# Performance work log

Measured on AMD Instinct MI355X. Metric: run time of the kernel, lower is better.

The kernel has to match this reference:

```python
import jax, jax.numpy as jnp
import numpy as np

B, I, O, K = 16384, 512, 64, 4


def setup_inputs() -> dict:
    key = jax.random.key(0)
    k1, k2, k3 = jax.random.split(key, 3)
    x = jax.random.normal(k1, (B, I), dtype=jnp.float32)
    weights = jax.random.normal(k2, (O, I), dtype=jnp.float32)
    # per-(o,i) Fourier coefficients, init like torch.randn * 0.1
    coefficients = jax.random.normal(k3, (O, I, 2 * K + 1), dtype=jnp.float32) * 0.1
    return {"x": x, "weights": weights, "coefficients": coefficients}


def reference(x, weights, coefficients):
    # x: [B, I]; weights: [O, I]; coefficients: [O, I, 2K+1]
    Kf = coefficients.shape[-1] // 2
    freqs = jnp.arange(1, Kf + 1, dtype=x.dtype)          # (k+1) for k in range(K)
    ang = x[:, :, None] * freqs                            # [B, I, K]
    sin_v = jnp.sin(ang)                                   # [B, I, K]
    cos_v = jnp.cos(ang)                                   # [B, I, K]
    c0 = coefficients[..., 0]                              # [O, I] constant term
    a = coefficients[..., 1::2]                            # [O, I, K] sin coeffs
    b = coefficients[..., 2::2]                            # [O, I, K] cos coeffs
    # out[b,o] = sum_i w[o,i] * (c0[o,i] + sum_k a*sin + b*cos)
    const = jnp.sum(weights * c0, axis=1)                  # [O]
    out = (const[None, :]
           + jnp.einsum('bik,oik->bo', sin_v, weights[:, :, None] * a)
           + jnp.einsum('bik,oik->bo', cos_v, weights[:, :, None] * b))
    return out
```

## Files before the change

kernel.cpp:

```cpp
#include <hip/hip_runtime.h>

#define B_ROWS 16384
#define I_DIM  512
#define O_DIM  64
#define NFEAT  8
#define W2_BYTES ((size_t)I_DIM * O_DIM * NFEAT * 2)

typedef _Float16 f16x8 __attribute__((ext_vector_type(8)));
typedef float    f32x4 __attribute__((ext_vector_type(4)));

__global__ __launch_bounds__(256) void prep_w2(const float* __restrict__ w,
                                               const float* __restrict__ coef,
                                               _Float16* __restrict__ w2) {
    int t = blockIdx.x * 256 + threadIdx.x;
    int i = t >> 6;
    int o = t & 63;
    float wv = w[o * I_DIM + i];
    const float* cp = coef + ((size_t)(o * I_DIM + i)) * 9;
    f16x8 v;
#pragma unroll
    for (int f = 0; f < 8; ++f) v[f] = (_Float16)(wv * cp[f + 1]);
    *reinterpret_cast<f16x8*>(w2 + (size_t)t * 8) = v;
}

__global__ __launch_bounds__(64) void prep_const(const float* __restrict__ w,
                                                 const float* __restrict__ coef,
                                                 float* __restrict__ cst) {
    int o = blockIdx.x;
    int l = threadIdx.x;
    float s = 0.f;
    for (int i = l; i < I_DIM; i += 64)
        s += w[o * I_DIM + i] * coef[((size_t)(o * I_DIM + i)) * 9];
#pragma unroll
    for (int off = 32; off; off >>= 1) s += __shfl_down(s, off, 64);
    if (l == 0) cst[o] = s;
}

__global__ __launch_bounds__(512) void fourier_main(const float* __restrict__ x,
                                                    const _Float16* __restrict__ w2,
                                                    const float* __restrict__ cst,
                                                    float* __restrict__ out) {
    __shared__ float red[4][64][64];

    const int tid   = threadIdx.x;
    const int wave  = tid >> 6;
    const int lane  = tid & 63;
    const int col16 = lane & 15;
    const int ig    = lane >> 4;
    const int rbase = blockIdx.x * 64;

    f32x4 acc[4][4] = {};
    const int i0 = wave * 64;

    const float* xr[4];
#pragma unroll
    for (int m = 0; m < 4; ++m)
        xr[m] = x + (size_t)(rbase + m * 16 + col16) * I_DIM;

    const f16x8* __restrict__ bbase = reinterpret_cast<const f16x8*>(w2);

    for (int s = 0; s < 16; ++s) {
        const int i = i0 + s * 4 + ig;

        f16x8 bf[4];
#pragma unroll
        for (int n = 0; n < 4; ++n) bf[n] = bbase[i * 64 + n * 16 + col16];

        float xv[4];
#pragma unroll
        for (int m = 0; m < 4; ++m) xv[m] = xr[m][i];

#pragma unroll
        for (int m = 0; m < 4; ++m) {
            float s1, c1;
            __sincosf(xv[m], &s1, &c1);
            const float tc = 2.f * c1;
            const float s2 = tc * s1;
            const float c2 = tc * c1 - 1.f;
            const float s3 = tc * s2 - s1;
            const float c3 = tc * c2 - c1;
            const float s4 = tc * s3 - s2;
            const float c4 = tc * c3 - c2;
            f16x8 af;
            af[0] = (_Float16)s1; af[1] = (_Float16)c1;
            af[2] = (_Float16)s2; af[3] = (_Float16)c2;
            af[4] = (_Float16)s3; af[5] = (_Float16)c3;
            af[6] = (_Float16)s4; af[7] = (_Float16)c4;
#pragma unroll
            for (int n = 0; n < 4; ++n)
                acc[m][n] = __builtin_amdgcn_mfma_f32_16x16x32_f16(af, bf[n], acc[m][n], 0, 0, 0);
        }
    }

    if (wave < 4) {
#pragma unroll
        for (int m = 0; m < 4; ++m)
#pragma unroll
            for (int n = 0; n < 4; ++n)
#pragma unroll
                for (int q = 0; q < 4; ++q)
                    red[wave][m * 16 + ig * 4 + q][n * 16 + col16] = acc[m][n][q];
    }
    __syncthreads();
    if (wave >= 4) {
#pragma unroll
        for (int m = 0; m < 4; ++m)
#pragma unroll
            for (int n = 0; n < 4; ++n)
#pragma unroll
                for (int q = 0; q < 4; ++q)
                    red[wave - 4][m * 16 + ig * 4 + q][n * 16 + col16] += acc[m][n][q];
    }
    __syncthreads();

    const float cv = cst[lane];
#pragma unroll
    for (int j = 0; j < 8; ++j) {
        const int r = wave + 8 * j;
        const int c = lane;
        float v = cv + red[0][r][c] + red[1][r][c] + red[2][r][c] + red[3][r][c];
        out[(size_t)(rbase + r) * 64 + c] = v;
    }
}

extern "C" void kernel_launch(void* const* d_in, const int* in_sizes, int n_in,
                              void* d_out, int out_size, void* d_ws, size_t ws_size,
                              hipStream_t stream) {
    const float* x    = (const float*)d_in[0];
    const float* w    = (const float*)d_in[1];
    const float* coef = (const float*)d_in[2];
    _Float16* w2  = (_Float16*)d_ws;
    float*    cst = (float*)((char*)d_ws + W2_BYTES);
    float*    out = (float*)d_out;

    hipLaunchKernelGGL(prep_w2,    dim3(128), dim3(256), 0, stream, w, coef, w2);
    hipLaunchKernelGGL(prep_const, dim3(64),  dim3(64),  0, stream, w, coef, cst);
    hipLaunchKernelGGL(fourier_main, dim3(B_ROWS / 64), dim3(512), 0, stream, x, w2, cst, out);
}
```

Baseline: 99.94 us.

## Stage x tile through shared memory with coalesced loads and prefetch weights

The main kernel now loads the block's 64x512 x tile with coalesced float4 global loads into registers. It writes the tile into a 128KB shared buffer in four row groups, and each wave reads its x values from shared memory instead of making strided per-row global loads. The loop order changes to row-group outer, with software prefetch of the next weight fragments. The reduction buffer reuses the x storage with padding. The prep kernels get coalesced reads and a wider reduction. The large shared allocation limits residency to one block per CU, and weight fragments are now reloaded for each row group, adding cache traffic.

```diff
diff --git a/kernel.cpp b/kernel.cpp
--- a/kernel.cpp
+++ b/kernel.cpp
@@ -13,34 +13,39 @@
                                                const float* __restrict__ coef,
                                                _Float16* __restrict__ w2) {
     int t = blockIdx.x * 256 + threadIdx.x;
-    int i = t >> 6;
-    int o = t & 63;
-    float wv = w[o * I_DIM + i];
-    const float* cp = coef + ((size_t)(o * I_DIM + i)) * 9;
+    int o = t >> 9;
+    int i = t & 511;
+    float wv = w[t];
+    const float* cp = coef + (size_t)t * 9;
     f16x8 v;
 #pragma unroll
     for (int f = 0; f < 8; ++f) v[f] = (_Float16)(wv * cp[f + 1]);
-    *reinterpret_cast<f16x8*>(w2 + (size_t)t * 8) = v;
+    *reinterpret_cast<f16x8*>(w2 + ((size_t)(i * 64 + o)) * 8) = v;
 }
 
-__global__ __launch_bounds__(64) void prep_const(const float* __restrict__ w,
-                                                 const float* __restrict__ coef,
-                                                 float* __restrict__ cst) {
+__global__ __launch_bounds__(256) void prep_const(const float* __restrict__ w,
+                                                  const float* __restrict__ coef,
+                                                  float* __restrict__ cst) {
     int o = blockIdx.x;
-    int l = threadIdx.x;
+    int t = threadIdx.x;
     float s = 0.f;
-    for (int i = l; i < I_DIM; i += 64)
+#pragma unroll
+    for (int i = t; i < I_DIM; i += 256)
         s += w[o * I_DIM + i] * coef[((size_t)(o * I_DIM + i)) * 9];
 #pragma unroll
     for (int off = 32; off; off >>= 1) s += __shfl_down(s, off, 64);
-    if (l == 0) cst[o] = s;
+    __shared__ float ps[4];
+    if ((t & 63) == 0) ps[t >> 6] = s;
+    __syncthreads();
+    if (t == 0) cst[o] = ps[0] + ps[1] + ps[2] + ps[3];
 }
 
-__global__ __launch_bounds__(512) void fourier_main(const float* __restrict__ x,
-                                                    const _Float16* __restrict__ w2,
-                                                    const float* __restrict__ cst,
-                                                    float* __restrict__ out) {
-    __shared__ float red[4][64][64];
+__global__ __launch_bounds__(512, 2) void fourier_main(const float* __restrict__ x,
+                                                       const _Float16* __restrict__ w2,
+                                                       const float* __restrict__ cst,
+                                                       float* __restrict__ out) {
+    __shared__ __align__(16) float xs[64][512];
+    float (*red)[64][65] = reinterpret_cast<float(*)[64][65]>(&xs[0][0]);
 
     const int tid   = threadIdx.x;
     const int wave  = tid >> 6;
@@ -48,32 +53,42 @@
     const int col16 = lane & 15;
     const int ig    = lane >> 4;
     const int rbase = blockIdx.x * 64;
+    const int i0    = wave * 64;
+
+    const float4* xg = reinterpret_cast<const float4*>(x + (size_t)rbase * I_DIM);
+    float4 xv16[16];
+#pragma unroll
+    for (int j = 0; j < 16; ++j) xv16[j] = xg[j * 512 + tid];
 
     f32x4 acc[4][4] = {};
-    const int i0 = wave * 64;
-
-    const float* xr[4];
-#pragma unroll
-    for (int m = 0; m < 4; ++m)
-        xr[m] = x + (size_t)(rbase + m * 16 + col16) * I_DIM;
-
     const f16x8* __restrict__ bbase = reinterpret_cast<const f16x8*>(w2);
 
-    for (int s = 0; s < 16; ++s) {
-        const int i = i0 + s * 4 + ig;
+#pragma unroll
+    for (int m = 0; m < 4; ++m) {
+#pragma unroll
+        for (int jj = 0; jj < 4; ++jj) {
+            const int j  = m * 4 + jj;
+            const int f4 = j * 512 + tid;
+            *reinterpret_cast<float4*>(&xs[f4 >> 7][(f4 & 127) << 2]) = xv16[j];
+        }
+        __syncthreads();
 
-        f16x8 bf[4];
+        f16x8 bf[4], bn[4];
+        {
+            const int i = i0 + ig;
 #pragma unroll
-        for (int n = 0; n < 4; ++n) bf[n] = bbase[i * 64 + n * 16 + col16];
-
-        float xv[4];
+            for (int n = 0; n < 4; ++n) bf[n] = bbase[i * 64 + n * 16 + col16];
+        }
+        for (int s = 0; s < 16; ++s) {
+            const int i = i0 + s * 4 + ig;
+            if (s < 15) {
+                const int i2 = i + 4;
 #pragma unroll
-        for (int m = 0; m < 4; ++m) xv[m] = xr[m][i];
-
-#pragma unroll
-        for (int m = 0; m < 4; ++m) {
+                for (int n = 0; n < 4; ++n) bn[n] = bbase[i2 * 64 + n * 16 + col16];
+            }
+            const float xv = xs[m * 16 + col16][i];
             float s1, c1;
-            __sincosf(xv[m], &s1, &c1);
+            __sincosf(xv, &s1, &c1);
             const float tc = 2.f * c1;
             const float s2 = tc * s1;
             const float c2 = tc * c1 - 1.f;
@@ -89,9 +104,12 @@
 #pragma unroll
             for (int n = 0; n < 4; ++n)
                 acc[m][n] = __builtin_amdgcn_mfma_f32_16x16x32_f16(af, bf[n], acc[m][n], 0, 0, 0);
+#pragma unroll
+            for (int n = 0; n < 4; ++n) bf[n] = bn[n];
         }
     }
 
+    __syncthreads();
     if (wave < 4) {
 #pragma unroll
         for (int m = 0; m < 4; ++m)
@@ -117,9 +135,8 @@
 #pragma unroll
     for (int j = 0; j < 8; ++j) {
         const int r = wave + 8 * j;
-        const int c = lane;
-        float v = cv + red[0][r][c] + red[1][r][c] + red[2][r][c] + red[3][r][c];
-        out[(size_t)(rbase + r) * 64 + c] = v;
+        float v = cv + red[0][r][lane] + red[1][r][lane] + red[2][r][lane] + red[3][r][lane];
+        out[(size_t)(rbase + r) * 64 + lane] = v;
     }
 }
 
@@ -134,6 +151,6 @@
     float*    out = (float*)d_out;
 
     hipLaunchKernelGGL(prep_w2,    dim3(128), dim3(256), 0, stream, w, coef, w2);
-    hipLaunchKernelGGL(prep_const, dim3(64),  dim3(64),  0, stream, w, coef, cst);
+    hipLaunchKernelGGL(prep_const, dim3(64),  dim3(256), 0, stream, w, coef, cst);
     hipLaunchKernelGGL(fourier_main, dim3(B_ROWS / 64), dim3(512), 0, stream, x, w2, cst, out);
 }
```

Result: slower. 111.6 us (+11.7%).
